# Kernel optimization log

Measured on AMD Instinct MI355X. Metric: run time of the kernel, lower is better.

Reference implementation:

```python
import jax, jax.numpy as jnp
import numpy as np

LN_EPS = 1e-5


def setup_inputs() -> dict:
    key = jax.random.key(0)
    ks = jax.random.split(key, 8)
    dim = 256
    b, n3 = 8, 6144  # seq dim holds 3 concatenated token streams of n=2048 each
    s = 0.02
    return {
        "x": jax.random.normal(ks[0], (b, n3, dim), jnp.float32),
        "ln_g": jnp.ones((dim,), jnp.float32),
        "ln_b": jnp.zeros((dim,), jnp.float32),
        "Wq": jax.random.normal(ks[1], (dim, dim), jnp.float32) * s,
        "bq": jax.random.normal(ks[2], (dim,), jnp.float32) * s,
        "Wk": jax.random.normal(ks[3], (dim, dim), jnp.float32) * s,
        "bk": jax.random.normal(ks[4], (dim,), jnp.float32) * s,
        "Wv": jax.random.normal(ks[5], (dim, dim), jnp.float32) * s,
        "bv": jax.random.normal(ks[6], (dim,), jnp.float32) * s,
        "Wo": jax.random.normal(ks[7], (dim, dim), jnp.float32) * s,
        "bo": jnp.zeros((dim,), jnp.float32),
        "heads": 8,
    }


def reference(x, ln_g, ln_b, Wq, bq, Wk, bk, Wv, bv, Wo, bo, heads):
    dim = x.shape[-1]
    scale = dim ** (-0.5)  # NOTE: full dim, as in the original module
    d = dim // heads

    def cross_attn(xcat):
        # LayerNorm over last dim (applied to concatenated [2b, n, dim])
        mu = jnp.mean(xcat, axis=-1, keepdims=True)
        var = jnp.mean(jnp.square(xcat - mu), axis=-1, keepdims=True)
        xn = (xcat - mu) * jax.lax.rsqrt(var + LN_EPS) * ln_g + ln_b
        x1, x2 = jnp.split(xn, 2, axis=0)  # queries from stream 1, kv from stream 2
        q = x1 @ Wq.T + bq
        k = x2 @ Wk.T + bk
        v = x2 @ Wv.T + bv
        b_, n_ = q.shape[0], q.shape[1]
        q = q.reshape(b_, n_, heads, d).transpose(0, 2, 1, 3)  # b h n d
        k = k.reshape(b_, n_, heads, d).transpose(0, 2, 1, 3)
        v = v.reshape(b_, n_, heads, d).transpose(0, 2, 1, 3)
        dots = jnp.einsum('bhid,bhjd->bhij', q, k) * scale
        attn = jax.nn.softmax(dots, axis=-1)
        out = jnp.einsum('bhij,bhjd->bhid', attn, v)
        out = out.transpose(0, 2, 1, 3).reshape(b_, n_, dim)
        return out @ Wo.T + bo  # dropout is identity in eval

    x_origin, x_emap, x_lbp = jnp.split(x, 3, axis=1)
    out_oe = cross_attn(jnp.concatenate((x_origin, x_emap), axis=0))
    out_ol = cross_attn(jnp.concatenate((x_origin, x_lbp), axis=0))
    return out_oe + out_ol
```

## Files before the change

kernel.cpp:

```cpp
#include <hip/hip_runtime.h>
#include <hip/hip_bf16.h>
#include <math.h>

#define LN_EPS 1e-5f
#define QSCALE 0.09016844005556021f

typedef __attribute__((ext_vector_type(8))) short short8;
typedef __attribute__((ext_vector_type(4))) short short4v;
typedef __attribute__((ext_vector_type(4))) float f32x4;

__device__ inline ushort f2bf(float f) {
  __hip_bfloat16 h = __float2bfloat16(f);
  return *reinterpret_cast<ushort*>(&h);
}

__device__ inline uint pk2bf(float a, float b) {
  uint ua = __float_as_uint(a) + 0x8000u;
  uint ub = __float_as_uint(b) + 0x8000u;
  return __builtin_amdgcn_perm(ub, ua, 0x07060302u);
}


__global__ __launch_bounds__(256) void ln_wcast_kernel(
    const float* __restrict__ x, const float* __restrict__ lng,
    const float* __restrict__ lnb,
    const float* __restrict__ Wq, const float* __restrict__ Wk,
    const float* __restrict__ Wv, const float* __restrict__ Wo,
    ushort* __restrict__ xn, ushort* __restrict__ wbf) {
  if (blockIdx.x < 256) {
    int t = blockIdx.x * 256 + threadIdx.x;
    int e0 = t * 4;
    int m = e0 >> 16, off = e0 & 65535;
    const float* src = (m == 0) ? Wq : (m == 1) ? Wk : (m == 2) ? Wv : Wo;
    float4 v = *(const float4*)(src + off);
    ushort4 o;
    o.x = f2bf(v.x); o.y = f2bf(v.y); o.z = f2bf(v.z); o.w = f2bf(v.w);
    *(ushort4*)(wbf + m * 65536 + off) = o;
    return;
  }
  int w = threadIdx.x >> 6;
  int lane = threadIdx.x & 63;
  size_t token = (size_t)(blockIdx.x - 256) * 4 + w;
  float4 v = *(const float4*)(x + token * 256 + lane * 4);
  float s  = v.x + v.y + v.z + v.w;
  float s2 = v.x * v.x + v.y * v.y + v.z * v.z + v.w * v.w;
#pragma unroll
  for (int off = 32; off >= 1; off >>= 1) {
    s  += __shfl_xor(s, off, 64);
    s2 += __shfl_xor(s2, off, 64);
  }
  float mu  = s * (1.0f / 256.0f);
  float var = s2 * (1.0f / 256.0f) - mu * mu;
  float rs  = rsqrtf(var + LN_EPS);
  float4 g = *(const float4*)(lng + lane * 4);
  float4 bb = *(const float4*)(lnb + lane * 4);
  ushort4 o;
  o.x = f2bf((v.x - mu) * rs * g.x + bb.x);
  o.y = f2bf((v.y - mu) * rs * g.y + bb.y);
  o.z = f2bf((v.z - mu) * rs * g.z + bb.z);
  o.w = f2bf((v.w - mu) * rs * g.w + bb.w);
  *(ushort4*)(xn + token * 256 + lane * 4) = o;
}

__global__ __launch_bounds__(256) void proj_kernel(
    const ushort* __restrict__ xn,
    const ushort* __restrict__ wq, const ushort* __restrict__ wk,
    const ushort* __restrict__ wv,
    const float* __restrict__ bq, const float* __restrict__ bk,
    const float* __restrict__ bv,
    ushort* __restrict__ qb, ushort* __restrict__ keb, ushort* __restrict__ vTe,
    ushort* __restrict__ klb, ushort* __restrict__ vTl) {
  int z = blockIdx.z;
  int tid = threadIdx.x;
  int w = tid >> 6, lane = tid & 63;
  int n = lane & 15, quad = lane >> 4;
  int cbase = blockIdx.y * 128 + w * 32;
  int b = (blockIdx.x * 128) >> 11;
  int r0 = (blockIdx.x * 128) & 2047;

  if (z == 0) {
    const ushort* xbase = xn + ((size_t)b * 6144 + r0) * 256;
    short8 wf[2][8];
#pragma unroll
    for (int ct = 0; ct < 2; ++ct)
#pragma unroll
      for (int kc = 0; kc < 8; ++kc)
        wf[ct][kc] = *(const short8*)(wq + (size_t)(cbase + ct * 16 + n) * 256 + kc * 32 + quad * 8);
    float4 bt[2];
    bt[0] = *(const float4*)(bq + cbase + quad * 4);
    bt[1] = *(const float4*)(bq + cbase + 16 + quad * 4);

    short8 xfA[8], xfB[8];
#pragma unroll
    for (int kc = 0; kc < 8; ++kc)
      xfA[kc] = *(const short8*)(xbase + (size_t)n * 256 + kc * 32 + quad * 8);

#pragma unroll
    for (int tt = 0; tt < 8; ++tt) {
      const short8* cur = (tt & 1) ? xfB : xfA;
      short8* nxt = (tt & 1) ? xfA : xfB;
      if (tt < 7) {
#pragma unroll
        for (int kc = 0; kc < 8; ++kc)
          nxt[kc] = *(const short8*)(xbase + (size_t)((tt + 1) * 16 + n) * 256 + kc * 32 + quad * 8);
      }
      f32x4 acc[2] = {{0.f, 0.f, 0.f, 0.f}, {0.f, 0.f, 0.f, 0.f}};
#pragma unroll
      for (int ct = 0; ct < 2; ++ct)
#pragma unroll
        for (int kc = 0; kc < 8; ++kc)
          acc[ct] = __builtin_amdgcn_mfma_f32_16x16x32_bf16(wf[ct][kc], cur[kc], acc[ct], 0, 0, 0);
      int n2 = r0 + tt * 16 + n;
#pragma unroll
      for (int ct = 0; ct < 2; ++ct) {
        int c = cbase + ct * 16 + quad * 4;
        int h = c >> 5, d = c & 31;
        float* bp = (float*)&bt[ct];
        ushort4 st;
        st.x = f2bf((acc[ct][0] + bp[0]) * QSCALE);
        st.y = f2bf((acc[ct][1] + bp[1]) * QSCALE);
        st.z = f2bf((acc[ct][2] + bp[2]) * QSCALE);
        st.w = f2bf((acc[ct][3] + bp[3]) * QSCALE);
        *(ushort4*)(qb + (((size_t)(b * 8 + h) * 2048) + n2) * 32 + d) = st;
      }
    }
  } else {
    int s = z;
    ushort* kout = (z == 1) ? keb : klb;
    ushort* vout = (z == 1) ? vTe : vTl;
    const ushort* xbase = xn + ((size_t)b * 6144 + s * 2048 + r0) * 256;
    short8 wfk[2][8], wfv[2][8];
#pragma unroll
    for (int ct = 0; ct < 2; ++ct)
#pragma unroll
      for (int kc = 0; kc < 8; ++kc) {
        wfk[ct][kc] = *(const short8*)(wk + (size_t)(cbase + ct * 16 + n) * 256 + kc * 32 + quad * 8);
        wfv[ct][kc] = *(const short8*)(wv + (size_t)(cbase + ct * 16 + n) * 256 + kc * 32 + quad * 8);
      }
    float4 btk[2];
    btk[0] = *(const float4*)(bk + cbase + quad * 4);
    btk[1] = *(const float4*)(bk + cbase + 16 + quad * 4);
    float bsv[2] = {bv[cbase + n], bv[cbase + 16 + n]};

    short8 xfA[8], xfB[8];
#pragma unroll
    for (int kc = 0; kc < 8; ++kc)
      xfA[kc] = *(const short8*)(xbase + (size_t)n * 256 + kc * 32 + quad * 8);

#pragma unroll
    for (int tt = 0; tt < 8; ++tt) {
      const short8* cur = (tt & 1) ? xfB : xfA;
      short8* nxt = (tt & 1) ? xfA : xfB;
      if (tt < 7) {
#pragma unroll
        for (int kc = 0; kc < 8; ++kc)
          nxt[kc] = *(const short8*)(xbase + (size_t)((tt + 1) * 16 + n) * 256 + kc * 32 + quad * 8);
      }
      f32x4 ack[2] = {{0.f, 0.f, 0.f, 0.f}, {0.f, 0.f, 0.f, 0.f}};
      f32x4 acv[2] = {{0.f, 0.f, 0.f, 0.f}, {0.f, 0.f, 0.f, 0.f}};
#pragma unroll
      for (int ct = 0; ct < 2; ++ct)
#pragma unroll
        for (int kc = 0; kc < 8; ++kc) {
          ack[ct] = __builtin_amdgcn_mfma_f32_16x16x32_bf16(wfk[ct][kc], cur[kc], ack[ct], 0, 0, 0);
          acv[ct] = __builtin_amdgcn_mfma_f32_16x16x32_bf16(cur[kc], wfv[ct][kc], acv[ct], 0, 0, 0);
        }
      int n2 = r0 + tt * 16 + n;
#pragma unroll
      for (int ct = 0; ct < 2; ++ct) {
        int c = cbase + ct * 16 + quad * 4;
        int h = c >> 5, d = c & 31;
        float* bp = (float*)&btk[ct];
        ushort4 st;
        st.x = f2bf(ack[ct][0] + bp[0]);
        st.y = f2bf(ack[ct][1] + bp[1]);
        st.z = f2bf(ack[ct][2] + bp[2]);
        st.w = f2bf(ack[ct][3] + bp[3]);
        *(ushort4*)(kout + (((size_t)(b * 8 + h) * 2048) + n2) * 32 + d) = st;
      }
      int tq = r0 + tt * 16 + quad * 4;
      int tile = tq >> 6;
      int t4 = (tq >> 4) & 3;
      int qp = (tq >> 2) & 3;
#pragma unroll
      for (int ct = 0; ct < 2; ++ct) {
        int c = cbase + ct * 16 + n;
        int h = c >> 5, d = c & 31;
        int dh = d >> 4, np = d & 15;
        ushort4 st;
        st.x = f2bf(acv[ct][0] + bsv[ct]);
        st.y = f2bf(acv[ct][1] + bsv[ct]);
        st.z = f2bf(acv[ct][2] + bsv[ct]);
        st.w = f2bf(acv[ct][3] + bsv[ct]);
        *(ushort4*)(vout + (size_t)(b * 8 + h) * 65536
                    + (size_t)((((tile * 2 + dh) * 4 + t4) * 64 + qp * 16 + np) * 4)) = st;
      }
    }
  }
}

__global__ __launch_bounds__(256, 4) void attn_kernel(
    const ushort* __restrict__ q,
    const ushort* __restrict__ ke, const ushort* __restrict__ vTe,
    const ushort* __restrict__ kl, const ushort* __restrict__ vTl,
    ushort* __restrict__ osum_e, ushort* __restrict__ osum_l) {
  int tid = threadIdx.x;
  int w = tid >> 6, lane = tid & 63;
  int n = lane & 15, quad = lane >> 4;

  union { uint2 u; short4v s; } one_u;
  one_u.u.x = 0x3F803F80u; one_u.u.y = 0x3F803F80u;
  const short4v vone = one_u.s;

  int L = blockIdx.y * 8 + blockIdx.x;
  int xcd = L & 7, idx = L >> 3;
  int bh = (idx >> 5) * 8 + xcd;
  int rem = idx & 31;
  int s = rem >> 4;
  int q0 = (rem & 15) * 128;
  int qbase = q0 + w * 32;

  const ushort* K  = (s == 0 ? ke : kl) + (size_t)bh * 2048 * 32;
  const ushort* VT = (s == 0 ? vTe : vTl) + (size_t)bh * 65536;
  ushort* osum = (s == 0) ? osum_e : osum_l;

  short8 qfrag[2];
#pragma unroll
  for (int gq = 0; gq < 2; ++gq)
    qfrag[gq] = *(const short8*)(q + ((size_t)bh * 2048 + qbase + gq * 16 + n) * 32 + quad * 8);

  f32x4 lacc[2];
  f32x4 oacc[2][2];
#pragma unroll
  for (int gq = 0; gq < 2; ++gq) {
    lacc[gq] = (f32x4){0.f, 0.f, 0.f, 0.f};
#pragma unroll
    for (int dh = 0; dh < 2; ++dh) oacc[gq][dh] = (f32x4){0.f, 0.f, 0.f, 0.f};
  }

  auto loadKV = [&](short8* kf, short4v (*vf)[4], int jt) {
    size_t tb = (size_t)jt * 2048;
#pragma unroll
    for (int t4 = 0; t4 < 4; ++t4)
      kf[t4] = *(const short8*)(K + tb + (size_t)(t4 * 16 + n) * 32 + quad * 8);
#pragma unroll
    for (int dh = 0; dh < 2; ++dh)
#pragma unroll
      for (int t4 = 0; t4 < 4; ++t4)
        vf[dh][t4] = *(const short4v*)(VT + tb + (dh * 4 + t4) * 256 + lane * 4);
  };

  auto compute = [&](const short8* kf, const short4v (*vf)[4]) {
#pragma unroll
    for (int gq = 0; gq < 2; ++gq) {
      f32x4 sacc[4];
#pragma unroll
      for (int t4 = 0; t4 < 4; ++t4) {
        f32x4 z = {0.f, 0.f, 0.f, 0.f};
        sacc[t4] = __builtin_amdgcn_mfma_f32_16x16x32_bf16(kf[t4], qfrag[gq], z, 0, 0, 0);
      }
      short4v pf[4];
#pragma unroll
      for (int t4 = 0; t4 < 4; ++t4) {
        float p0 = __builtin_amdgcn_exp2f(sacc[t4][0]);
        float p1 = __builtin_amdgcn_exp2f(sacc[t4][1]);
        float p2 = __builtin_amdgcn_exp2f(sacc[t4][2]);
        float p3 = __builtin_amdgcn_exp2f(sacc[t4][3]);
        union { uint2 u; short4v s4; } cv;
        cv.u.x = pk2bf(p0, p1);
        cv.u.y = pk2bf(p2, p3);
        pf[t4] = cv.s4;
      }
#pragma unroll
      for (int t4 = 0; t4 < 4; ++t4) {
        oacc[gq][0] = __builtin_amdgcn_mfma_f32_16x16x16bf16_1k(pf[t4], vf[0][t4], oacc[gq][0], 0, 0, 0);
        oacc[gq][1] = __builtin_amdgcn_mfma_f32_16x16x16bf16_1k(pf[t4], vf[1][t4], oacc[gq][1], 0, 0, 0);
        lacc[gq]    = __builtin_amdgcn_mfma_f32_16x16x16bf16_1k(pf[t4], vone, lacc[gq], 0, 0, 0);
      }
    }
  };

  short8 kfA[4], kfB[4];
  short4v vfA[2][4], vfB[2][4];
  loadKV(kfA, vfA, 0);
  for (int jt = 0; jt < 32; jt += 2) {
    loadKV(kfB, vfB, jt + 1);
    compute(kfA, vfA);
    if (jt + 2 < 32) loadKV(kfA, vfA, jt + 2);
    compute(kfB, vfB);
  }

  int b = bh >> 3, h = bh & 7;
#pragma unroll
  for (int gq = 0; gq < 2; ++gq) {
    f32x4 inv;
#pragma unroll
    for (int r = 0; r < 4; ++r) inv[r] = __builtin_amdgcn_rcpf(lacc[gq][r]);
#pragma unroll
    for (int dh = 0; dh < 2; ++dh) {
      f32x4 v = oacc[gq][dh] * inv;
#pragma unroll
      for (int r = 0; r < 4; ++r) {
        size_t row = (size_t)b * 2048 + qbase + gq * 16 + quad * 4 + r;
        osum[row * 256 + h * 32 + dh * 16 + n] = f2bf(v[r]);
      }
    }
  }
}

__global__ __launch_bounds__(256) void outproj_kernel(
    const ushort* __restrict__ ose, const ushort* __restrict__ osl,
    const ushort* __restrict__ wo,
    const float* __restrict__ bo, float* __restrict__ out) {
  int tid = threadIdx.x;
  int w = tid >> 6, lane = tid & 63;
  int n = lane & 15, quad = lane >> 4;
  int cbase = blockIdx.y * 128 + w * 32;

  short8 wfrag[2][8];
#pragma unroll
  for (int ct = 0; ct < 2; ++ct)
#pragma unroll
    for (int kc = 0; kc < 8; ++kc)
      wfrag[ct][kc] = *(const short8*)(wo + (size_t)(cbase + ct * 16 + n) * 256 + kc * 32 + quad * 8);
  float4 bt[2];
  bt[0] = *(const float4*)(bo + cbase + quad * 4);
  bt[1] = *(const float4*)(bo + cbase + 16 + quad * 4);

  const ushort* ae = ose + (size_t)(blockIdx.x * 64) * 256;
  const ushort* al = osl + (size_t)(blockIdx.x * 64) * 256;

#pragma unroll
  for (int tt = 0; tt < 4; ++tt) {
    short8 xe[8], xl[8];
#pragma unroll
    for (int kc = 0; kc < 8; ++kc)
      xe[kc] = *(const short8*)(ae + (size_t)(tt * 16 + n) * 256 + kc * 32 + quad * 8);
#pragma unroll
    for (int kc = 0; kc < 8; ++kc)
      xl[kc] = *(const short8*)(al + (size_t)(tt * 16 + n) * 256 + kc * 32 + quad * 8);

    int tok = blockIdx.x * 64 + tt * 16 + n;
    f32x4 acc[2] = {{0.f, 0.f, 0.f, 0.f}, {0.f, 0.f, 0.f, 0.f}};
#pragma unroll
    for (int ct = 0; ct < 2; ++ct)
#pragma unroll
      for (int kc = 0; kc < 8; ++kc)
        acc[ct] = __builtin_amdgcn_mfma_f32_16x16x32_bf16(wfrag[ct][kc], xe[kc], acc[ct], 0, 0, 0);
#pragma unroll
    for (int ct = 0; ct < 2; ++ct)
#pragma unroll
      for (int kc = 0; kc < 8; ++kc)
        acc[ct] = __builtin_amdgcn_mfma_f32_16x16x32_bf16(wfrag[ct][kc], xl[kc], acc[ct], 0, 0, 0);
#pragma unroll
    for (int ct = 0; ct < 2; ++ct) {
      int c = cbase + ct * 16 + quad * 4;
      float* bp = (float*)&bt[ct];
      float4 st;
      st.x = acc[ct][0] + 2.0f * bp[0];
      st.y = acc[ct][1] + 2.0f * bp[1];
      st.z = acc[ct][2] + 2.0f * bp[2];
      st.w = acc[ct][3] + 2.0f * bp[3];
      *(float4*)(out + (size_t)tok * 256 + c) = st;
    }
  }
}

extern "C" void kernel_launch(void* const* d_in, const int* in_sizes, int n_in,
                              void* d_out, int out_size, void* d_ws, size_t ws_size,
                              hipStream_t stream) {
  const float* x   = (const float*)d_in[0];
  const float* lng = (const float*)d_in[1];
  const float* lnb = (const float*)d_in[2];
  const float* Wq  = (const float*)d_in[3];
  const float* bq  = (const float*)d_in[4];
  const float* Wk  = (const float*)d_in[5];
  const float* bk  = (const float*)d_in[6];
  const float* Wv  = (const float*)d_in[7];
  const float* bv  = (const float*)d_in[8];
  const float* Wo  = (const float*)d_in[9];
  const float* bo  = (const float*)d_in[10];
  float* out = (float*)d_out;

  ushort* ws = (ushort*)d_ws;
  const size_t XN  = (size_t)49152 * 256;
  const size_t QKV = (size_t)64 * 2048 * 32;
  ushort* xn     = ws;
  ushort* wbf    = xn + XN;
  ushort* qb     = wbf + 4 * 65536;
  ushort* keb    = qb  + QKV;
  ushort* vTe    = keb + QKV;
  ushort* klb    = vTe + QKV;
  ushort* vTl    = klb + QKV;
  ushort* osum_e = vTl + QKV;
  ushort* osum_l = xn;

  hipLaunchKernelGGL(ln_wcast_kernel, dim3(12544), dim3(256), 0, stream,
                     x, lng, lnb, Wq, Wk, Wv, Wo, xn, wbf);
  hipLaunchKernelGGL(proj_kernel, dim3(128, 2, 3), dim3(256), 0, stream,
                     xn, wbf, wbf + 65536, wbf + 131072, bq, bk, bv,
                     qb, keb, vTe, klb, vTl);
  hipLaunchKernelGGL(attn_kernel, dim3(8, 256), dim3(256), 0, stream,
                     qb, keb, vTe, klb, vTl, osum_e, osum_l);
  hipLaunchKernelGGL(outproj_kernel, dim3(256, 2), dim3(256), 0, stream,
                     osum_e, osum_l, wbf + 196608, bo, out);
}
```

Baseline: 293.9 us.

## Switch attention inner loop to 32x32x16 MFMA with row-sum via shuffles

Rewrites the attention kernel to use 32x32x16 bf16 MFMAs for both the QK^T scores and the PV product, so each wave handles 32 queries by 64 keys per tile with fewer, larger instructions. The softmax denominator is now summed with VALU adds and a cross-lane shuffle, replacing the extra ones-vector MFMA. The V projection store layout is changed to match the new operand fragment layout, and s_setprio is placed around the MFMA groups. The larger accumulators raise register use, so the occupancy hint drops from 4 to 3 waves per SIMD.

```diff
diff --git a/kernel.cpp b/kernel.cpp
--- a/kernel.cpp
+++ b/kernel.cpp
@@ -8,6 +8,7 @@
 typedef __attribute__((ext_vector_type(8))) short short8;
 typedef __attribute__((ext_vector_type(4))) short short4v;
 typedef __attribute__((ext_vector_type(4))) float f32x4;
+typedef __attribute__((ext_vector_type(16))) float f32x16;
 
 __device__ inline ushort f2bf(float f) {
   __hip_bfloat16 h = __float2bfloat16(f);
@@ -179,38 +180,36 @@
         *(ushort4*)(kout + (((size_t)(b * 8 + h) * 2048) + n2) * 32 + d) = st;
       }
       int tq = r0 + tt * 16 + quad * 4;
-      int tile = tq >> 6;
-      int t4 = (tq >> 4) & 3;
-      int qp = (tq >> 2) & 3;
+      int ktile = tq >> 5;
+      int u = (tq >> 4) & 1;
+      int i0 = 4 * (quad >> 1);
+      int hi2 = quad & 1;
 #pragma unroll
       for (int ct = 0; ct < 2; ++ct) {
         int c = cbase + ct * 16 + n;
-        int h = c >> 5, d = c & 31;
-        int dh = d >> 4, np = d & 15;
+        int h = c >> 5;
+        int d = ct * 16 + n;
+        int lane2 = d + 32 * hi2;
         ushort4 st;
         st.x = f2bf(acv[ct][0] + bsv[ct]);
         st.y = f2bf(acv[ct][1] + bsv[ct]);
         st.z = f2bf(acv[ct][2] + bsv[ct]);
         st.w = f2bf(acv[ct][3] + bsv[ct]);
         *(ushort4*)(vout + (size_t)(b * 8 + h) * 65536
-                    + (size_t)((((tile * 2 + dh) * 4 + t4) * 64 + qp * 16 + np) * 4)) = st;
+                    + ktile * 1024 + u * 512 + lane2 * 8 + i0) = st;
       }
     }
   }
 }
 
-__global__ __launch_bounds__(256, 4) void attn_kernel(
+__global__ __launch_bounds__(256, 3) void attn_kernel(
     const ushort* __restrict__ q,
     const ushort* __restrict__ ke, const ushort* __restrict__ vTe,
     const ushort* __restrict__ kl, const ushort* __restrict__ vTl,
     ushort* __restrict__ osum_e, ushort* __restrict__ osum_l) {
   int tid = threadIdx.x;
   int w = tid >> 6, lane = tid & 63;
-  int n = lane & 15, quad = lane >> 4;
-
-  union { uint2 u; short4v s; } one_u;
-  one_u.u.x = 0x3F803F80u; one_u.u.y = 0x3F803F80u;
-  const short4v vone = one_u.s;
+  int l31 = lane & 31, hi = lane >> 5;
 
   int L = blockIdx.y * 8 + blockIdx.x;
   int xcd = L & 7, idx = L >> 3;
@@ -220,68 +219,68 @@
   int q0 = (rem & 15) * 128;
   int qbase = q0 + w * 32;
 
-  const ushort* K  = (s == 0 ? ke : kl) + (size_t)bh * 2048 * 32;
+  const ushort* K  = (s == 0 ? ke : kl) + (size_t)bh * 65536;
   const ushort* VT = (s == 0 ? vTe : vTl) + (size_t)bh * 65536;
   ushort* osum = (s == 0) ? osum_e : osum_l;
 
-  short8 qfrag[2];
-#pragma unroll
-  for (int gq = 0; gq < 2; ++gq)
-    qfrag[gq] = *(const short8*)(q + ((size_t)bh * 2048 + qbase + gq * 16 + n) * 32 + quad * 8);
-
-  f32x4 lacc[2];
-  f32x4 oacc[2][2];
-#pragma unroll
-  for (int gq = 0; gq < 2; ++gq) {
-    lacc[gq] = (f32x4){0.f, 0.f, 0.f, 0.f};
-#pragma unroll
-    for (int dh = 0; dh < 2; ++dh) oacc[gq][dh] = (f32x4){0.f, 0.f, 0.f, 0.f};
-  }
-
-  auto loadKV = [&](short8* kf, short4v (*vf)[4], int jt) {
-    size_t tb = (size_t)jt * 2048;
-#pragma unroll
-    for (int t4 = 0; t4 < 4; ++t4)
-      kf[t4] = *(const short8*)(K + tb + (size_t)(t4 * 16 + n) * 32 + quad * 8);
-#pragma unroll
-    for (int dh = 0; dh < 2; ++dh)
-#pragma unroll
-      for (int t4 = 0; t4 < 4; ++t4)
-        vf[dh][t4] = *(const short4v*)(VT + tb + (dh * 4 + t4) * 256 + lane * 4);
+  short8 qf[2];
+#pragma unroll
+  for (int sl = 0; sl < 2; ++sl)
+    qf[sl] = *(const short8*)(q + ((size_t)bh * 2048 + qbase + l31) * 32 + sl * 16 + hi * 8);
+
+  f32x16 oacc;
+#pragma unroll
+  for (int r = 0; r < 16; ++r) oacc[r] = 0.f;
+  float lsum = 0.f;
+
+  auto loadKV = [&](short8* kf, short8* vf, int jt) {
+    const ushort* kb = K + (size_t)jt * 2048;
+#pragma unroll
+    for (int kt = 0; kt < 2; ++kt)
+#pragma unroll
+      for (int sl = 0; sl < 2; ++sl)
+        kf[kt * 2 + sl] = *(const short8*)(kb + (kt * 32 + l31) * 32 + sl * 16 + hi * 8);
+    const ushort* vb = VT + (size_t)jt * 2048 + lane * 8;
+#pragma unroll
+    for (int m = 0; m < 4; ++m)
+      vf[m] = *(const short8*)(vb + m * 512);
   };
 
-  auto compute = [&](const short8* kf, const short4v (*vf)[4]) {
-#pragma unroll
-    for (int gq = 0; gq < 2; ++gq) {
-      f32x4 sacc[4];
-#pragma unroll
-      for (int t4 = 0; t4 < 4; ++t4) {
-        f32x4 z = {0.f, 0.f, 0.f, 0.f};
-        sacc[t4] = __builtin_amdgcn_mfma_f32_16x16x32_bf16(kf[t4], qfrag[gq], z, 0, 0, 0);
-      }
-      short4v pf[4];
-#pragma unroll
-      for (int t4 = 0; t4 < 4; ++t4) {
-        float p0 = __builtin_amdgcn_exp2f(sacc[t4][0]);
-        float p1 = __builtin_amdgcn_exp2f(sacc[t4][1]);
-        float p2 = __builtin_amdgcn_exp2f(sacc[t4][2]);
-        float p3 = __builtin_amdgcn_exp2f(sacc[t4][3]);
-        union { uint2 u; short4v s4; } cv;
-        cv.u.x = pk2bf(p0, p1);
-        cv.u.y = pk2bf(p2, p3);
-        pf[t4] = cv.s4;
-      }
-#pragma unroll
-      for (int t4 = 0; t4 < 4; ++t4) {
-        oacc[gq][0] = __builtin_amdgcn_mfma_f32_16x16x16bf16_1k(pf[t4], vf[0][t4], oacc[gq][0], 0, 0, 0);
-        oacc[gq][1] = __builtin_amdgcn_mfma_f32_16x16x16bf16_1k(pf[t4], vf[1][t4], oacc[gq][1], 0, 0, 0);
-        lacc[gq]    = __builtin_amdgcn_mfma_f32_16x16x16bf16_1k(pf[t4], vone, lacc[gq], 0, 0, 0);
-      }
+  auto compute = [&](const short8* kf, const short8* vf) {
+#pragma unroll
+    for (int kt = 0; kt < 2; ++kt) {
+      f32x16 sacc;
+#pragma unroll
+      for (int r = 0; r < 16; ++r) sacc[r] = 0.f;
+      __builtin_amdgcn_s_setprio(1);
+      sacc = __builtin_amdgcn_mfma_f32_32x32x16_bf16(kf[kt * 2 + 0], qf[0], sacc, 0, 0, 0);
+      sacc = __builtin_amdgcn_mfma_f32_32x32x16_bf16(kf[kt * 2 + 1], qf[1], sacc, 0, 0, 0);
+      __builtin_amdgcn_s_setprio(0);
+      float p[16];
+#pragma unroll
+      for (int r = 0; r < 16; ++r) p[r] = __builtin_amdgcn_exp2f(sacc[r]);
+      float ps = 0.f;
+#pragma unroll
+      for (int r = 0; r < 16; ++r) ps += p[r];
+      lsum += ps;
+      short8 pa[2];
+#pragma unroll
+      for (int u = 0; u < 2; ++u) {
+        union { uint4 uu; short8 s8; } cv;
+        cv.uu.x = pk2bf(p[8 * u + 0], p[8 * u + 1]);
+        cv.uu.y = pk2bf(p[8 * u + 2], p[8 * u + 3]);
+        cv.uu.z = pk2bf(p[8 * u + 4], p[8 * u + 5]);
+        cv.uu.w = pk2bf(p[8 * u + 6], p[8 * u + 7]);
+        pa[u] = cv.s8;
+      }
+      __builtin_amdgcn_s_setprio(1);
+      oacc = __builtin_amdgcn_mfma_f32_32x32x16_bf16(pa[0], vf[kt * 2 + 0], oacc, 0, 0, 0);
+      oacc = __builtin_amdgcn_mfma_f32_32x32x16_bf16(pa[1], vf[kt * 2 + 1], oacc, 0, 0, 0);
+      __builtin_amdgcn_s_setprio(0);
     }
   };
 
-  short8 kfA[4], kfB[4];
-  short4v vfA[2][4], vfB[2][4];
+  short8 kfA[4], kfB[4], vfA[4], vfB[4];
   loadKV(kfA, vfA, 0);
   for (int jt = 0; jt < 32; jt += 2) {
     loadKV(kfB, vfB, jt + 1);
@@ -290,21 +289,17 @@
     compute(kfB, vfB);
   }
 
+  lsum += __shfl_xor(lsum, 32, 64);
+  float inv = __builtin_amdgcn_rcpf(lsum);
+
   int b = bh >> 3, h = bh & 7;
 #pragma unroll
-  for (int gq = 0; gq < 2; ++gq) {
-    f32x4 inv;
-#pragma unroll
-    for (int r = 0; r < 4; ++r) inv[r] = __builtin_amdgcn_rcpf(lacc[gq][r]);
-#pragma unroll
-    for (int dh = 0; dh < 2; ++dh) {
-      f32x4 v = oacc[gq][dh] * inv;
-#pragma unroll
-      for (int r = 0; r < 4; ++r) {
-        size_t row = (size_t)b * 2048 + qbase + gq * 16 + quad * 4 + r;
-        osum[row * 256 + h * 32 + dh * 16 + n] = f2bf(v[r]);
-      }
-    }
+  for (int r = 0; r < 16; ++r) {
+    int qr = (r & 3) + 8 * (r >> 2) + 4 * hi;
+    float invr = __shfl(inv, qr, 64);
+    float v = oacc[r] * invr;
+    size_t row = (size_t)b * 2048 + qbase + qr;
+    osum[row * 256 + h * 32 + l31] = f2bf(v);
   }
 }
 
```

Result: faster. 271.6 us (-7.6%).
